# Kernel optimization log

Hardware: AMD Instinct MI355X
Metric: run time of the kernel (lower is better)

Reference implementation:

```python
import jax, jax.numpy as jnp
import numpy as np

N_NODES = 1_000_000   # nodal points, 3 DOFs each
N_ELEMS = 500_000     # H8 (8-node hexahedral) elements
N_TYPES = 64          # distinct element stiffness matrices (24x24)


def setup_inputs() -> dict:
    key = jax.random.key(0)
    k1, k2, k3, k4 = jax.random.split(key, 4)
    U = jax.random.normal(k1, (N_NODES, 3), dtype=jnp.float32)
    filters = jax.random.normal(k2, (N_TYPES, 24, 24), dtype=jnp.float32)
    H8types = jax.random.randint(k3, (N_ELEMS,), 0, N_TYPES, dtype=jnp.int32)
    nodIdx = jax.random.randint(k4, (N_ELEMS, 8), 0, N_NODES, dtype=jnp.int32)
    return {"U": U, "filters": filters, "H8types": H8types, "nodIdx": nodIdx}


def reference(U, filters, H8types, nodIdx):
    """FEM stiffness matvec KU = sum_e scatter(K_type(e) @ gather(U, e)).

    U:       [N, 3]      nodal displacements (3 DOFs per node)
    filters: [T, 24, 24] per-type element stiffness matrices
    H8types: [E]         element type index into filters
    nodIdx:  [E, 8]      element -> node connectivity
    returns KU: [N, 3]
    """
    E = nodIdx.shape[0]
    # gather the 8 nodes x 3 DOFs of each element -> [E, 24]
    ue = U[nodIdx].reshape(E, 24)
    # per-type stiffness for each element -> [E, 24, 24]
    Ke = filters[H8types]
    # per-element force vector f_e = K_e @ u_e -> [E, 24]
    fe = jnp.einsum('eij,ej->ei', Ke, ue)
    # scatter-add element forces back to nodal DOFs
    KU = jnp.zeros_like(U).at[nodIdx.reshape(-1)].add(fe.reshape(E * 8, 3))
    return KU
```

## Files before the change

### kernel.cpp

```cpp
#include <hip/hip_runtime.h>


#define NTYPES    64
#define KSTRIDE   580
#define RSHIFT    11
#define RNODES    2048
#define MAXB      512
#define CAP       10240
#define K1_TPB    1024
#define K1_EPT    2
#define K1_CHUNK  (K1_TPB * K1_EPT)
#define K2_TPB    256
#define PREP_TPB  256

typedef int          nint4  __attribute__((ext_vector_type(4)));
typedef unsigned int nuint2 __attribute__((ext_vector_type(2)));
typedef unsigned int nuint4 __attribute__((ext_vector_type(4)));

__device__ __forceinline__ unsigned bf16_rne(float f) {
    unsigned b = __float_as_uint(f);
    return (b + 0x7FFFu + ((b >> 16) & 1u)) >> 16;
}


__global__ __launch_bounds__(PREP_TPB) void pack_u_kernel(
    const float* __restrict__ U, nuint2* __restrict__ Ub,
    float* __restrict__ KU, unsigned* __restrict__ tails,
    int n_nodes, int n_buckets)
{
    int n = blockIdx.x * PREP_TPB + threadIdx.x;
    if (n < n_buckets) tails[n] = 0;
    if (n >= n_nodes) return;
    const float* up = U + (size_t)n * 3;
    unsigned bx = bf16_rne(up[0]);
    unsigned by = bf16_rne(up[1]);
    unsigned bz = bf16_rne(up[2]);
    nuint2 v = { bx | (by << 16), bz };
    Ub[n] = v;
    KU[3 * n + 0] = 0.f;
    KU[3 * n + 1] = 0.f;
    KU[3 * n + 2] = 0.f;
}


__global__ __launch_bounds__(K1_TPB, 4) void feconv_bin_kernel(
    const nuint2* __restrict__ Ub,
    const float* __restrict__ K,
    const int*   __restrict__ types,
    const int*   __restrict__ nodIdx,
    float*       __restrict__ KU,
    unsigned*    __restrict__ tails,
    nuint2*      __restrict__ recs,
    int n_elems, int n_buckets)
{
    extern __shared__ float sK[];
    __shared__ unsigned sCnt[MAXB];
    __shared__ unsigned sBase[MAXB];

    for (int w = threadIdx.x; w < NTYPES * 576; w += K1_TPB) {
        int t = w / 576;
        int r = w - t * 576;
        sK[t * KSTRIDE + r] = K[w];
    }
    for (int i = threadIdx.x; i < n_buckets; i += K1_TPB) sCnt[i] = 0;
    __syncthreads();

    const int e0 = blockIdx.x * K1_CHUNK + threadIdx.x;
    int     nodes[K1_EPT][8];
    int     tt[K1_EPT];
    nuint2  uu[K1_EPT][8];

#pragma unroll
    for (int k = 0; k < K1_EPT; ++k) {
        int e = e0 + k * K1_TPB;
        tt[k] = -1;
        if (e < n_elems) {
            tt[k] = __builtin_nontemporal_load(&types[e]);
            const nint4* q = (const nint4*)(nodIdx + (size_t)e * 8);
            nint4 a = __builtin_nontemporal_load(q);
            nint4 b = __builtin_nontemporal_load(q + 1);
            nodes[k][0] = a.x; nodes[k][1] = a.y; nodes[k][2] = a.z; nodes[k][3] = a.w;
            nodes[k][4] = b.x; nodes[k][5] = b.y; nodes[k][6] = b.z; nodes[k][7] = b.w;
#pragma unroll
            for (int j = 0; j < 8; ++j)
                uu[k][j] = Ub[nodes[k][j]];
#pragma unroll
            for (int j = 0; j < 8; ++j)
                atomicAdd(&sCnt[(unsigned)nodes[k][j] >> RSHIFT], 1u);
        }
    }
    __syncthreads();

    for (int b = threadIdx.x; b < n_buckets; b += K1_TPB) {
        unsigned c = sCnt[b];
        sBase[b] = c ? atomicAdd(&tails[b], c) : 0u;
        sCnt[b] = 0;
    }
    __syncthreads();

#pragma unroll
    for (int k = 0; k < K1_EPT; ++k) {
        if (tt[k] < 0) continue;

        float ue[24];
#pragma unroll
        for (int j = 0; j < 8; ++j) {
            nuint2 v = uu[k][j];
            ue[3 * j + 0] = __uint_as_float(v.x << 16);
            ue[3 * j + 1] = __uint_as_float(v.x & 0xFFFF0000u);
            ue[3 * j + 2] = __uint_as_float(v.y << 16);
        }

        const float4* Kt4 = (const float4*)(sK + tt[k] * KSTRIDE);
#pragma unroll
        for (int j = 0; j < 8; ++j) {
            float a0 = 0.f, a1 = 0.f, a2 = 0.f;
#pragma unroll
            for (int q = 0; q < 6; ++q) {
                float4 k0 = Kt4[(3 * j + 0) * 6 + q];
                float4 k1 = Kt4[(3 * j + 1) * 6 + q];
                float4 k2 = Kt4[(3 * j + 2) * 6 + q];
                float u0 = ue[4 * q + 0], u1 = ue[4 * q + 1];
                float u2 = ue[4 * q + 2], u3 = ue[4 * q + 3];
                a0 += k0.x * u0 + k0.y * u1 + k0.z * u2 + k0.w * u3;
                a1 += k1.x * u0 + k1.y * u1 + k1.z * u2 + k1.w * u3;
                a2 += k2.x * u0 + k2.y * u1 + k2.z * u2 + k2.w * u3;
            }
            unsigned n = (unsigned)nodes[k][j];
            unsigned b = n >> RSHIFT;
            unsigned pos = sBase[b] + atomicAdd(&sCnt[b], 1u);
            if (pos < CAP) {
                unsigned local = n & (RNODES - 1);
                nuint2 r = { bf16_rne(a0) | (bf16_rne(a1) << 16),
                             bf16_rne(a2) | (local << 16) };
                recs[(size_t)b * CAP + pos] = r;
            } else {
                atomicAdd(&KU[(size_t)n * 3 + 0], a0);
                atomicAdd(&KU[(size_t)n * 3 + 1], a1);
                atomicAdd(&KU[(size_t)n * 3 + 2], a2);
            }
        }
    }
}


__global__ __launch_bounds__(K2_TPB) void feconv_acc_kernel(
    const nuint2*   __restrict__ recs,
    const unsigned* __restrict__ tails,
    float*          __restrict__ KU,
    int n_nodes)
{
    __shared__ float sAcc[RNODES * 3];
    const int b = blockIdx.x;

    for (int i = threadIdx.x; i < RNODES * 3; i += K2_TPB) sAcc[i] = 0.f;
    __syncthreads();

    unsigned cnt = tails[b];
    if (cnt > CAP) cnt = CAP;
    const nuint2* base = recs + (size_t)b * CAP;
    const nuint4* base4 = (const nuint4*)base;

    unsigned npairs = cnt >> 1;
    for (unsigned i = threadIdx.x; i < npairs; i += K2_TPB) {
        nuint4 p = base4[i];
        unsigned o0 = (p.y >> 16) * 3;
        atomicAdd(&sAcc[o0 + 0], __uint_as_float(p.x << 16));
        atomicAdd(&sAcc[o0 + 1], __uint_as_float(p.x & 0xFFFF0000u));
        atomicAdd(&sAcc[o0 + 2], __uint_as_float(p.y << 16));
        unsigned o1 = (p.w >> 16) * 3;
        atomicAdd(&sAcc[o1 + 0], __uint_as_float(p.z << 16));
        atomicAdd(&sAcc[o1 + 1], __uint_as_float(p.z & 0xFFFF0000u));
        atomicAdd(&sAcc[o1 + 2], __uint_as_float(p.w << 16));
    }
    if ((cnt & 1u) && threadIdx.x == 0) {
        nuint2 r = base[cnt - 1];
        unsigned o = (r.y >> 16) * 3;
        atomicAdd(&sAcc[o + 0], __uint_as_float(r.x << 16));
        atomicAdd(&sAcc[o + 1], __uint_as_float(r.x & 0xFFFF0000u));
        atomicAdd(&sAcc[o + 2], __uint_as_float(r.y << 16));
    }
    __syncthreads();

    const int nbase = b * RNODES;
    int limit = n_nodes - nbase;
    if (limit > RNODES) limit = RNODES;
    limit *= 3;
    float* out = KU + (size_t)nbase * 3;
    for (int i = threadIdx.x; i < limit; i += K2_TPB) out[i] += sAcc[i];
}


__global__ __launch_bounds__(256) void feconv_elem_kernel(
    const float* __restrict__ U, const float* __restrict__ K,
    const int* __restrict__ types, const int* __restrict__ nodIdx,
    float* __restrict__ KU, int n_elems)
{
    int e = blockIdx.x * blockDim.x + threadIdx.x;
    if (e >= n_elems) return;
    int t = types[e];
    const int4* idx4 = (const int4*)(nodIdx + (size_t)e * 8);
    int4 iA = idx4[0], iB = idx4[1];
    int nodes[8] = {iA.x, iA.y, iA.z, iA.w, iB.x, iB.y, iB.z, iB.w};
    float ue[24];
#pragma unroll
    for (int j = 0; j < 8; ++j) {
        const float* up = U + (size_t)nodes[j] * 3;
        ue[3 * j + 0] = up[0]; ue[3 * j + 1] = up[1]; ue[3 * j + 2] = up[2];
    }
    const float* Kt = K + (size_t)t * 576;
#pragma unroll
    for (int i = 0; i < 24; ++i) {
        const float4* row = (const float4*)(Kt + i * 24);
        float acc = 0.f;
#pragma unroll
        for (int q = 0; q < 6; ++q) {
            float4 k = row[q];
            acc += k.x * ue[4 * q + 0] + k.y * ue[4 * q + 1]
                 + k.z * ue[4 * q + 2] + k.w * ue[4 * q + 3];
        }
        atomicAdd(&KU[(size_t)nodes[i / 3] * 3 + (i % 3)], acc);
    }
}

extern "C" void kernel_launch(void* const* d_in, const int* in_sizes, int n_in,
                              void* d_out, int out_size, void* d_ws, size_t ws_size,
                              hipStream_t stream) {
    const float* U      = (const float*)d_in[0];
    const float* Kf     = (const float*)d_in[1];
    const int*   types  = (const int*)d_in[2];
    const int*   nodIdx = (const int*)d_in[3];
    float*       KU     = (float*)d_out;

    const int n_elems = in_sizes[2];
    const int n_nodes = in_sizes[0] / 3;
    const int n_buckets = (n_nodes + RNODES - 1) / RNODES;

    const size_t ub_off  = 4096;
    const size_t rec_off = ub_off + (((size_t)n_nodes * 8 + 255) & ~255ull);
    const size_t need    = rec_off + (size_t)n_buckets * CAP * 8;

    if (n_buckets <= MAXB && ws_size >= need) {
        unsigned* tails = (unsigned*)d_ws;
        nuint2*   Ub    = (nuint2*)((char*)d_ws + ub_off);
        nuint2*   recs  = (nuint2*)((char*)d_ws + rec_off);

        int gridP = (n_nodes + PREP_TPB - 1) / PREP_TPB;
        pack_u_kernel<<<gridP, PREP_TPB, 0, stream>>>(
            U, Ub, KU, tails, n_nodes, n_buckets);

        size_t lds_bytes = (size_t)NTYPES * KSTRIDE * sizeof(float);
        int grid1 = (n_elems + K1_CHUNK - 1) / K1_CHUNK;
        feconv_bin_kernel<<<grid1, K1_TPB, lds_bytes, stream>>>(
            Ub, Kf, types, nodIdx, KU, tails, recs, n_elems, n_buckets);
        feconv_acc_kernel<<<n_buckets, K2_TPB, 0, stream>>>(
            recs, tails, KU, n_nodes);
    } else {
        (void)hipMemsetAsync(KU, 0, (size_t)out_size * sizeof(float), stream);
        int block = 256;
        int grid = (n_elems + block - 1) / block;
        feconv_elem_kernel<<<grid, block, 0, stream>>>(
            U, Kf, types, nodIdx, KU, n_elems);
    }
}
```

Baseline: 215.5 us.

## Sort elements by type so each block loads only one stiffness matrix

Adds a binning pass that groups element ids by type into per-type lists, then launches compute blocks per (type, chunk). Each block loads a single 24x24 matrix into LDS instead of all 64 (about 148 KB per block), which allows smaller blocks and higher occupancy. In exchange there is an extra kernel launch, an indirect elemIds lookup, and nodIdx reads that are no longer coalesced. Many blocks exit early because each type gets a fixed capacity of 20 chunks. Elements beyond the per-type capacity fall back to a direct fp32 atomic path.

```diff
diff --git a/kernel.cpp b/kernel.cpp
--- a/kernel.cpp
+++ b/kernel.cpp
@@ -2,16 +2,17 @@
 
 
 #define NTYPES    64
-#define KSTRIDE   580
 #define RSHIFT    11
 #define RNODES    2048
 #define MAXB      512
 #define CAP       10240
-#define K1_TPB    1024
-#define K1_EPT    2
-#define K1_CHUNK  (K1_TPB * K1_EPT)
+#define TCAP      10240
+#define K1_TPB    512
+#define K1_CHUNK  K1_TPB
+#define CHUNKS    (TCAP / K1_CHUNK)
 #define K2_TPB    256
 #define PREP_TPB  256
+#define BIN_TPB   256
 
 typedef int          nint4  __attribute__((ext_vector_type(4)));
 typedef unsigned int nuint2 __attribute__((ext_vector_type(2)));
@@ -22,14 +23,45 @@
     return (b + 0x7FFFu + ((b >> 16) & 1u)) >> 16;
 }
 
+__device__ void elem_direct(const float* __restrict__ U,
+                            const float* __restrict__ K,
+                            const int* __restrict__ nodIdx,
+                            float* __restrict__ KU, int e, int t)
+{
+    const int4* idx4 = (const int4*)(nodIdx + (size_t)e * 8);
+    int4 iA = idx4[0], iB = idx4[1];
+    int nodes[8] = {iA.x, iA.y, iA.z, iA.w, iB.x, iB.y, iB.z, iB.w};
+    float ue[24];
+#pragma unroll
+    for (int j = 0; j < 8; ++j) {
+        const float* up = U + (size_t)nodes[j] * 3;
+        ue[3 * j + 0] = up[0]; ue[3 * j + 1] = up[1]; ue[3 * j + 2] = up[2];
+    }
+    const float* Kt = K + (size_t)t * 576;
+#pragma unroll
+    for (int i = 0; i < 24; ++i) {
+        const float4* row = (const float4*)(Kt + i * 24);
+        float acc = 0.f;
+#pragma unroll
+        for (int q = 0; q < 6; ++q) {
+            float4 k = row[q];
+            acc += k.x * ue[4 * q + 0] + k.y * ue[4 * q + 1]
+                 + k.z * ue[4 * q + 2] + k.w * ue[4 * q + 3];
+        }
+        atomicAdd(&KU[(size_t)nodes[i / 3] * 3 + (i % 3)], acc);
+    }
+}
+
 
 __global__ __launch_bounds__(PREP_TPB) void pack_u_kernel(
     const float* __restrict__ U, nuint2* __restrict__ Ub,
     float* __restrict__ KU, unsigned* __restrict__ tails,
+    unsigned* __restrict__ typeTails,
     int n_nodes, int n_buckets)
 {
     int n = blockIdx.x * PREP_TPB + threadIdx.x;
     if (n < n_buckets) tails[n] = 0;
+    if (n < NTYPES) typeTails[n] = 0;
     if (n >= n_nodes) return;
     const float* up = U + (size_t)n * 3;
     unsigned bx = bf16_rne(up[0]);
@@ -43,51 +75,85 @@
 }
 
 
-__global__ __launch_bounds__(K1_TPB, 4) void feconv_bin_kernel(
+__global__ __launch_bounds__(BIN_TPB) void bin_elems_kernel(
+    const int* __restrict__ types,
+    int* __restrict__ elemIds,
+    unsigned* __restrict__ typeTails,
+    const float* __restrict__ U, const float* __restrict__ Kf,
+    const int* __restrict__ nodIdx, float* __restrict__ KU,
+    int n_elems)
+{
+    __shared__ unsigned tCnt[NTYPES];
+    __shared__ unsigned tBase[NTYPES];
+    if (threadIdx.x < NTYPES) tCnt[threadIdx.x] = 0;
+    __syncthreads();
+
+    int e = blockIdx.x * BIN_TPB + threadIdx.x;
+    int t = -1; unsigned pos = 0;
+    if (e < n_elems) {
+        t = __builtin_nontemporal_load(&types[e]);
+        pos = atomicAdd(&tCnt[t], 1u);
+    }
+    __syncthreads();
+
+    if (threadIdx.x < NTYPES) {
+        unsigned c = tCnt[threadIdx.x];
+        tBase[threadIdx.x] = c ? atomicAdd(&typeTails[threadIdx.x], c) : 0u;
+    }
+    __syncthreads();
+
+    if (t >= 0) {
+        unsigned p = tBase[t] + pos;
+        if (p < TCAP) elemIds[(size_t)t * TCAP + p] = e;
+        else elem_direct(U, Kf, nodIdx, KU, e, t);
+    }
+}
+
+
+__global__ __launch_bounds__(K1_TPB, 8) void feconv_bin_kernel(
     const nuint2* __restrict__ Ub,
-    const float* __restrict__ K,
-    const int*   __restrict__ types,
-    const int*   __restrict__ nodIdx,
-    float*       __restrict__ KU,
-    unsigned*    __restrict__ tails,
-    nuint2*      __restrict__ recs,
-    int n_elems, int n_buckets)
-{
-    extern __shared__ float sK[];
+    const float*  __restrict__ K,
+    const int*    __restrict__ elemIds,
+    const unsigned* __restrict__ typeTails,
+    const int*    __restrict__ nodIdx,
+    float*        __restrict__ KU,
+    unsigned*     __restrict__ tails,
+    nuint2*       __restrict__ recs,
+    int n_buckets)
+{
+    __shared__ float    sK[576];
     __shared__ unsigned sCnt[MAXB];
     __shared__ unsigned sBase[MAXB];
 
-    for (int w = threadIdx.x; w < NTYPES * 576; w += K1_TPB) {
-        int t = w / 576;
-        int r = w - t * 576;
-        sK[t * KSTRIDE + r] = K[w];
-    }
+    const int t = blockIdx.x / CHUNKS;
+    const unsigned start = (unsigned)(blockIdx.x % CHUNKS) * K1_CHUNK;
+    unsigned cnt = typeTails[t];
+    if (cnt > TCAP) cnt = TCAP;
+    if (start >= cnt) return;
+
+    if (threadIdx.x < 144)
+        ((float4*)sK)[threadIdx.x] =
+            ((const float4*)(K + (size_t)t * 576))[threadIdx.x];
     for (int i = threadIdx.x; i < n_buckets; i += K1_TPB) sCnt[i] = 0;
     __syncthreads();
 
-    const int e0 = blockIdx.x * K1_CHUNK + threadIdx.x;
-    int     nodes[K1_EPT][8];
-    int     tt[K1_EPT];
-    nuint2  uu[K1_EPT][8];
-
-#pragma unroll
-    for (int k = 0; k < K1_EPT; ++k) {
-        int e = e0 + k * K1_TPB;
-        tt[k] = -1;
-        if (e < n_elems) {
-            tt[k] = __builtin_nontemporal_load(&types[e]);
-            const nint4* q = (const nint4*)(nodIdx + (size_t)e * 8);
-            nint4 a = __builtin_nontemporal_load(q);
-            nint4 b = __builtin_nontemporal_load(q + 1);
-            nodes[k][0] = a.x; nodes[k][1] = a.y; nodes[k][2] = a.z; nodes[k][3] = a.w;
-            nodes[k][4] = b.x; nodes[k][5] = b.y; nodes[k][6] = b.z; nodes[k][7] = b.w;
-#pragma unroll
-            for (int j = 0; j < 8; ++j)
-                uu[k][j] = Ub[nodes[k][j]];
-#pragma unroll
-            for (int j = 0; j < 8; ++j)
-                atomicAdd(&sCnt[(unsigned)nodes[k][j] >> RSHIFT], 1u);
-        }
+    int    e = -1;
+    int    nodes[8];
+    nuint2 uu[8];
+    const unsigned li = start + threadIdx.x;
+    if (li < cnt) {
+        e = elemIds[(size_t)t * TCAP + li];
+        const nint4* q = (const nint4*)(nodIdx + (size_t)e * 8);
+        nint4 a = q[0];
+        nint4 b = q[1];
+        nodes[0] = a.x; nodes[1] = a.y; nodes[2] = a.z; nodes[3] = a.w;
+        nodes[4] = b.x; nodes[5] = b.y; nodes[6] = b.z; nodes[7] = b.w;
+#pragma unroll
+        for (int j = 0; j < 8; ++j)
+            uu[j] = Ub[nodes[j]];
+#pragma unroll
+        for (int j = 0; j < 8; ++j)
+            atomicAdd(&sCnt[(unsigned)nodes[j] >> RSHIFT], 1u);
     }
     __syncthreads();
 
@@ -98,20 +164,17 @@
     }
     __syncthreads();
 
-#pragma unroll
-    for (int k = 0; k < K1_EPT; ++k) {
-        if (tt[k] < 0) continue;
-
+    if (e >= 0) {
         float ue[24];
 #pragma unroll
         for (int j = 0; j < 8; ++j) {
-            nuint2 v = uu[k][j];
+            nuint2 v = uu[j];
             ue[3 * j + 0] = __uint_as_float(v.x << 16);
             ue[3 * j + 1] = __uint_as_float(v.x & 0xFFFF0000u);
             ue[3 * j + 2] = __uint_as_float(v.y << 16);
         }
 
-        const float4* Kt4 = (const float4*)(sK + tt[k] * KSTRIDE);
+        const float4* Kt4 = (const float4*)sK;
 #pragma unroll
         for (int j = 0; j < 8; ++j) {
             float a0 = 0.f, a1 = 0.f, a2 = 0.f;
@@ -126,7 +189,7 @@
                 a1 += k1.x * u0 + k1.y * u1 + k1.z * u2 + k1.w * u3;
                 a2 += k2.x * u0 + k2.y * u1 + k2.z * u2 + k2.w * u3;
             }
-            unsigned n = (unsigned)nodes[k][j];
+            unsigned n = (unsigned)nodes[j];
             unsigned b = n >> RSHIFT;
             unsigned pos = sBase[b] + atomicAdd(&sCnt[b], 1u);
             if (pos < CAP) {
@@ -199,28 +262,7 @@
     int e = blockIdx.x * blockDim.x + threadIdx.x;
     if (e >= n_elems) return;
     int t = types[e];
-    const int4* idx4 = (const int4*)(nodIdx + (size_t)e * 8);
-    int4 iA = idx4[0], iB = idx4[1];
-    int nodes[8] = {iA.x, iA.y, iA.z, iA.w, iB.x, iB.y, iB.z, iB.w};
-    float ue[24];
-#pragma unroll
-    for (int j = 0; j < 8; ++j) {
-        const float* up = U + (size_t)nodes[j] * 3;
-        ue[3 * j + 0] = up[0]; ue[3 * j + 1] = up[1]; ue[3 * j + 2] = up[2];
-    }
-    const float* Kt = K + (size_t)t * 576;
-#pragma unroll
-    for (int i = 0; i < 24; ++i) {
-        const float4* row = (const float4*)(Kt + i * 24);
-        float acc = 0.f;
-#pragma unroll
-        for (int q = 0; q < 6; ++q) {
-            float4 k = row[q];
-            acc += k.x * ue[4 * q + 0] + k.y * ue[4 * q + 1]
-                 + k.z * ue[4 * q + 2] + k.w * ue[4 * q + 3];
-        }
-        atomicAdd(&KU[(size_t)nodes[i / 3] * 3 + (i % 3)], acc);
-    }
+    elem_direct(U, K, nodIdx, KU, e, t);
 }
 
 extern "C" void kernel_launch(void* const* d_in, const int* in_sizes, int n_in,
@@ -238,21 +280,28 @@
 
     const size_t ub_off  = 4096;
     const size_t rec_off = ub_off + (((size_t)n_nodes * 8 + 255) & ~255ull);
-    const size_t need    = rec_off + (size_t)n_buckets * CAP * 8;
+    const size_t eid_off = rec_off + (size_t)n_buckets * CAP * 8;
+    const size_t need    = eid_off + (size_t)NTYPES * TCAP * 4;
 
     if (n_buckets <= MAXB && ws_size >= need) {
-        unsigned* tails = (unsigned*)d_ws;
-        nuint2*   Ub    = (nuint2*)((char*)d_ws + ub_off);
-        nuint2*   recs  = (nuint2*)((char*)d_ws + rec_off);
+        unsigned* tails     = (unsigned*)d_ws;
+        unsigned* typeTails = (unsigned*)((char*)d_ws + 2048);
+        nuint2*   Ub        = (nuint2*)((char*)d_ws + ub_off);
+        nuint2*   recs      = (nuint2*)((char*)d_ws + rec_off);
+        int*      elemIds   = (int*)((char*)d_ws + eid_off);
 
         int gridP = (n_nodes + PREP_TPB - 1) / PREP_TPB;
         pack_u_kernel<<<gridP, PREP_TPB, 0, stream>>>(
-            U, Ub, KU, tails, n_nodes, n_buckets);
-
-        size_t lds_bytes = (size_t)NTYPES * KSTRIDE * sizeof(float);
-        int grid1 = (n_elems + K1_CHUNK - 1) / K1_CHUNK;
-        feconv_bin_kernel<<<grid1, K1_TPB, lds_bytes, stream>>>(
-            Ub, Kf, types, nodIdx, KU, tails, recs, n_elems, n_buckets);
+            U, Ub, KU, tails, typeTails, n_nodes, n_buckets);
+
+        int gridB = (n_elems + BIN_TPB - 1) / BIN_TPB;
+        bin_elems_kernel<<<gridB, BIN_TPB, 0, stream>>>(
+            types, elemIds, typeTails, U, Kf, nodIdx, KU, n_elems);
+
+        int grid1 = NTYPES * CHUNKS;
+        feconv_bin_kernel<<<grid1, K1_TPB, 0, stream>>>(
+            Ub, Kf, elemIds, typeTails, nodIdx, KU, tails, recs, n_buckets);
+
         feconv_acc_kernel<<<n_buckets, K2_TPB, 0, stream>>>(
             recs, tails, KU, n_nodes);
     } else {
```

Result: slower. 360.4 us (+67.3%).
